# Kernel tuning notes

Measured on AMD Instinct MI355X. Metric: run time of the kernel, lower is better.

The kernel has to match this reference:

```python
import jax, jax.numpy as jnp
import numpy as np

B, NPG = 128, 128          # graphs, nodes per graph
N = B * NPG                # total nodes
K = 16                     # kNN neighbors within cutoff
D = 256                    # embedding_depth
H, DH = 4, 32              # heads = num_layers, head dim = (D//2)//H
L = 4                      # num graph convolutions
NR = 50                    # num_radial
CUTOFF = 2.0
OUT = 3 + 100              # 3 + max_ntypes


def setup_inputs() -> dict:
    rng = np.random.default_rng(0)
    pos = rng.standard_normal((N, 3)).astype(np.float32)
    nbrs = np.zeros((N, K), np.int32)
    mask = np.zeros((N, K), np.float32)
    for g in range(B):  # per-graph kNN with radial cutoff (setup only, numpy)
        p = pos[g * NPG:(g + 1) * NPG]
        d2 = ((p[:, None, :] - p[None, :, :]) ** 2).sum(-1)
        np.fill_diagonal(d2, np.inf)
        idx = np.argsort(d2, axis=1)[:, :K]
        dk = np.sqrt(np.take_along_axis(d2, idx, 1))
        nbrs[g * NPG:(g + 1) * NPG] = idx + g * NPG
        mask[g * NPG:(g + 1) * NPG] = (dk <= CUTOFF).astype(np.float32)
    batch_idx = np.repeat(np.arange(B, dtype=np.int32), NPG)

    key = jax.random.key(0)
    ks = jax.random.split(key, 12)
    s = 0.02
    return {
        'encoding': jax.random.normal(ks[0], (B, D), jnp.float32),
        'pos': jnp.asarray(pos),
        'batch_idx': jnp.asarray(batch_idx),
        'neighbors': jnp.asarray(nbrs),
        'nbr_mask': jnp.asarray(mask),
        'W_in': jax.random.normal(ks[1], (D + 3, D), jnp.float32) * s,
        'b_in': jnp.zeros((D,), jnp.float32),
        'Wq': jax.random.normal(ks[2], (L, D, H * DH), jnp.float32) * s,
        'Wk': jax.random.normal(ks[3], (L, D, H * DH), jnp.float32) * s,
        'Wv': jax.random.normal(ks[4], (L, D, H * DH), jnp.float32) * s,
        'We': jax.random.normal(ks[5], (L, NR, H * DH), jnp.float32) * s,
        'Wo': jax.random.normal(ks[6], (L, H * DH, D), jnp.float32) * s,
        'bo': jnp.zeros((L, D), jnp.float32),
        'Wfc': jax.random.normal(ks[7], (L, D, D), jnp.float32) * s,
        'bfc': jnp.zeros((L, D), jnp.float32),
        'ln_g': jnp.ones((L, D), jnp.float32),
        'ln_b': jnp.zeros((L, D), jnp.float32),
        'W_out': jax.random.normal(ks[8], (D, OUT), jnp.float32) * s,
        'b_out': jnp.zeros((OUT,), jnp.float32),
    }


def reference(encoding, pos, batch_idx, neighbors, nbr_mask,
              W_in, b_in, Wq, Wk, Wv, We, Wo, bo, Wfc, bfc,
              ln_g, ln_b, W_out, b_out):
    # x = encoding.repeat_interleave(graph_sizes); x[:, 0] = 1
    x = encoding[batch_idx]                      # [N, D]
    x = x.at[:, 0].set(1.0)
    h = jnp.concatenate([x, pos], axis=-1) @ W_in + b_in   # concat pos, embed

    # gaussian radial basis of neighbor distances
    dvec = pos[neighbors] - pos[:, None, :]      # [N, K, 3]
    d = jnp.sqrt((dvec ** 2).sum(-1) + 1e-12)    # [N, K]
    centers = jnp.linspace(0.0, CUTOFF, NR)
    width = centers[1] - centers[0]
    rbf = jnp.exp(-0.5 * ((d[..., None] - centers) / width) ** 2)  # [N, K, NR]

    scale = 1.0 / jnp.sqrt(jnp.float32(DH))
    m = nbr_mask[..., None]                      # [N, K, 1]
    for l in range(L):                           # TransformerConv layers
        q = (h @ Wq[l]).reshape(N, H, DH)
        k = (h @ Wk[l]).reshape(N, H, DH)
        v = (h @ Wv[l]).reshape(N, H, DH)
        e = (rbf @ We[l]).reshape(N, K, H, DH)   # edge embedding
        kj = k[neighbors] + e                    # [N, K, H, DH]
        vj = v[neighbors] + e
        logits = jnp.einsum('nhd,nkhd->nkh', q, kj) * scale
        logits = jnp.where(m > 0, logits, -1e9)
        a = jax.nn.softmax(logits, axis=1) * m   # masked attention over K
        msg = jnp.einsum('nkh,nkhd->nhd', a, vj).reshape(N, H * DH)
        h = h + msg @ Wo[l] + bo[l]              # residual update
        mu = h.mean(-1, keepdims=True)
        var = h.var(-1, keepdims=True)
        h = ln_g[l] * (h - mu) / jnp.sqrt(var + 1e-5) + ln_b[l]
        h = jax.nn.gelu(h @ Wfc[l] + bfc[l])     # nodewise fc (1 layer)

    return h @ W_out + b_out                     # [N, 3 + max_ntypes]
```

## Files before the change

### kernel.cpp

```cpp
#include <hip/hip_runtime.h>
#include <hip/hip_bf16.h>
#include <math.h>

#define N_PTS 16384
#define NLAYER 4

typedef __attribute__((ext_vector_type(8))) short bfrag;
typedef __attribute__((ext_vector_type(4))) float f32x4;
typedef __attribute__((ext_vector_type(4))) unsigned short u16x4;
typedef unsigned short ushort_t;
typedef unsigned int uint_t;

__device__ __forceinline__ ushort_t f2b(float f) {
  __hip_bfloat16 h = __float2bfloat16(f);
  return *reinterpret_cast<const ushort_t*>(&h);
}
__device__ __forceinline__ float b2f(ushort_t u) {
  union { uint_t i; float f; } c; c.i = ((uint_t)u) << 16; return c.f;
}
__device__ __forceinline__ float blo(uint_t u) {
  union { uint_t i; float f; } c; c.i = u << 16; return c.f;
}
__device__ __forceinline__ float bhi(uint_t u) {
  union { uint_t i; float f; } c; c.i = u & 0xffff0000u; return c.f;
}

__device__ __forceinline__ void gload16(const ushort_t* g, ushort_t* l) {
  __builtin_amdgcn_global_load_lds(
      (const __attribute__((address_space(1))) unsigned int*)g,
      (__attribute__((address_space(3))) unsigned int*)l, 16, 0, 0);
}

__global__ __launch_bounds__(256) void base_kernel(
    const float* __restrict__ enc, const float* __restrict__ W_in,
    const float* __restrict__ b_in, float* __restrict__ base)
{
  int b = blockIdx.x, j = threadIdx.x;
  __shared__ float se[256];
  se[j] = enc[b * 256 + j];
  __syncthreads();
  float acc = b_in[j] + W_in[j];
  for (int i = 1; i < 256; ++i) acc += se[i] * W_in[i * 256 + j];
  base[b * 256 + j] = acc;
}

__global__ __launch_bounds__(256) void embed_kernel(
    const float* __restrict__ base, const int* __restrict__ batch_idx,
    const float* __restrict__ pos, const float* __restrict__ W_in,
    float* __restrict__ h, ushort_t* __restrict__ h_bf)
{
  int n = blockIdx.x, j = threadIdx.x;
  int b = batch_idx[n];
  float px = pos[n * 3 + 0], py = pos[n * 3 + 1], pz = pos[n * 3 + 2];
  float v = base[b * 256 + j]
      + px * W_in[256 * 256 + j] + py * W_in[257 * 256 + j] + pz * W_in[258 * 256 + j];
  h[(size_t)n * 256 + j] = v;
  h_bf[(size_t)n * 256 + j] = f2b(v);
}

__global__ __launch_bounds__(256) void prep_qkv(
    const float* __restrict__ Wq, const float* __restrict__ Wk,
    const float* __restrict__ Wv, const float* __restrict__ We,
    ushort_t* __restrict__ out)
{
  int idx = blockIdx.x * 256 + threadIdx.x;
  int l = idx / (640 * 256);
  int rem = idx - l * (640 * 256);
  int j = rem >> 8, k = rem & 255;
  float v = 0.f;
  if (j < 128) v = Wq[((size_t)l * 256 + k) * 128 + j];
  else if (j < 328) {
    int p = j - 128, hq = p / 50, r = p - hq * 50;
    const float* wq = &Wq[((size_t)l * 256 + k) * 128 + hq * 32];
    const float* we = &We[((size_t)l * 50 + r) * 128 + hq * 32];
#pragma unroll
    for (int d = 0; d < 32; ++d) v += wq[d] * we[d];
  } else if (j < 456) v = Wk[((size_t)l * 256 + k) * 128 + (j - 328)];
  else if (j < 584) v = Wv[((size_t)l * 256 + k) * 128 + (j - 456)];
  out[idx] = f2b(v);
}

__global__ __launch_bounds__(256) void prep_bcat(
    const float* __restrict__ We, const float* __restrict__ Wo, ushort_t* __restrict__ out)
{
  int idx = blockIdx.x * 256 + threadIdx.x;
  int l = idx / (256 * 384);
  int rem = idx - l * (256 * 384);
  int j = rem / 384, k2 = rem - j * 384;
  float v = 0.f;
  if (k2 < 128) v = Wo[((size_t)l * 128 + k2) * 256 + j];
  else if (k2 < 328) {
    int p = k2 - 128, hq = p / 50, r = p - hq * 50;
    const float* we = &We[((size_t)l * 50 + r) * 128 + hq * 32];
    const float* wo = &Wo[((size_t)l * 128 + hq * 32) * 256 + j];
#pragma unroll
    for (int d = 0; d < 32; ++d) v += we[d] * wo[(size_t)d * 256];
  }
  out[idx] = f2b(v);
}

__global__ __launch_bounds__(256) void prep_wfc(
    const float* __restrict__ Wfc, ushort_t* __restrict__ out)
{
  int idx = blockIdx.x * 256 + threadIdx.x;
  int l = idx >> 16, rem = idx & 65535;
  int j = rem >> 8, k = rem & 255;
  out[idx] = f2b(Wfc[((size_t)l * 256 + k) * 256 + j]);
}

__global__ __launch_bounds__(256) void prep_wout(
    const float* __restrict__ W_out, ushort_t* __restrict__ out)
{
  int idx = blockIdx.x * 256 + threadIdx.x;
  int j = idx >> 8, k = idx & 255;
  out[idx] = (j < 103) ? f2b(W_out[(size_t)k * 103 + j]) : (ushort_t)0;
}

template<int MODE>
__global__ __launch_bounds__(512, 2) void fused_layer(
    const ushort_t* __restrict__ A0,
    const ushort_t* __restrict__ BcT,
    const float* __restrict__ bo,
    float* __restrict__ h,
    const float* __restrict__ lg, const float* __restrict__ lb,
    const ushort_t* __restrict__ WfT,
    const float* __restrict__ bfc,
    const ushort_t* __restrict__ W3T,
    const float* __restrict__ b3,
    ushort_t* __restrict__ qext_b, ushort_t* __restrict__ kvb,
    float* __restrict__ outF)
{
  __shared__ __align__(16) ushort_t R0[64 * 392];
  __shared__ __align__(16) ushort_t R12[64 * 264 + 256 * 64];
  __shared__ float pS[8][64], pSS[8][64];
  ushort_t* sA  = R0;
  ushort_t* sHg = R0;
  ushort_t* sH  = R12;
  ushort_t* sB  = R12 + 64 * 264;
  ushort_t* B3  = R12;

  const int tid = threadIdx.x;
  const int lane = tid & 63, w = tid >> 6;
  const int l15 = lane & 15, l4 = lane >> 4;
  const int m0 = blockIdx.x * 64;
  const int swzk = (l15 & 7) << 3;

  f32x4 acc[4][2];

  if constexpr (MODE != 2) {
    for (int i = tid; i < 64 * 48; i += 512) {
      int r = i / 48, cc = (i - r * 48) * 8;
      uint4 v = (uint4){0, 0, 0, 0};
      if (cc < 352) v = *(const uint4*)(A0 + (size_t)(m0 + r) * 352 + cc);
      *(uint4*)(&sA[r * 392 + cc]) = v;
    }

#pragma unroll
    for (int m = 0; m < 4; ++m) {
      acc[m][0] = (f32x4){0.f, 0.f, 0.f, 0.f};
      acc[m][1] = (f32x4){0.f, 0.f, 0.f, 0.f};
    }
    for (int ks = 0; ks < 6; ++ks) {
      const int k0 = ks * 64;
#pragma unroll
      for (int it = 0; it < 4; ++it) {
        int chunk = it * 512 + tid;
        int row = chunk >> 3;
        int kc = ((chunk & 7) << 3) ^ ((row & 7) << 3);
        gload16(BcT + (size_t)row * 384 + k0 + kc, sB + (size_t)(it * 512 + w * 64) * 8);
      }
      __syncthreads();
#pragma unroll
      for (int kk = 0; kk < 64; kk += 32) {
        bfrag af[4], bf[2];
#pragma unroll
        for (int m = 0; m < 4; ++m)
          af[m] = *(const bfrag*)(sA + (m * 16 + l15) * 392 + k0 + kk + l4 * 8);
#pragma unroll
        for (int nn = 0; nn < 2; ++nn) {
          int row = w * 32 + nn * 16 + l15;
          bf[nn] = *(const bfrag*)(sB + row * 64 + ((kk + l4 * 8) ^ swzk));
        }
#pragma unroll
        for (int m = 0; m < 4; ++m)
#pragma unroll
          for (int nn = 0; nn < 2; ++nn)
            acc[m][nn] = __builtin_amdgcn_mfma_f32_16x16x32_bf16(af[m], bf[nn], acc[m][nn], 0, 0, 0);
      }
      __syncthreads();
    }

    {
      const int c0 = w * 32 + l15, c1 = c0 + 16;
      const float bo0 = bo[c0], bo1 = bo[c1];
#pragma unroll
      for (int m = 0; m < 4; ++m)
#pragma unroll
        for (int i = 0; i < 4; ++i) {
          const int rl = m * 16 + l4 * 4 + i;
          const size_t r = (size_t)(m0 + rl);
          float x0 = acc[m][0][i] + bo0 + h[r * 256 + c0];
          float x1 = acc[m][1][i] + bo1 + h[r * 256 + c1];
          acc[m][0][i] = x0; acc[m][1][i] = x1;
          float s = x0 + x1, ss = x0 * x0 + x1 * x1;
          s += __shfl_xor(s, 1, 64); ss += __shfl_xor(ss, 1, 64);
          s += __shfl_xor(s, 2, 64); ss += __shfl_xor(ss, 2, 64);
          s += __shfl_xor(s, 4, 64); ss += __shfl_xor(ss, 4, 64);
          s += __shfl_xor(s, 8, 64); ss += __shfl_xor(ss, 8, 64);
          if (l15 == 0) { pS[w][rl] = s; pSS[w][rl] = ss; }
        }
      __syncthreads();
      const float g0 = lg[c0], g1 = lg[c1];
      const float b0 = lb[c0], b1 = lb[c1];
#pragma unroll
      for (int m = 0; m < 4; ++m)
#pragma unroll
        for (int i = 0; i < 4; ++i) {
          const int rl = m * 16 + l4 * 4 + i;
          float s = 0.f, ss = 0.f;
#pragma unroll
          for (int w2 = 0; w2 < 8; ++w2) { s += pS[w2][rl]; ss += pSS[w2][rl]; }
          float mu = s * (1.f / 256.f);
          float var = ss * (1.f / 256.f) - mu * mu;
          float inv = 1.0f / sqrtf(var + 1e-5f);
          sH[rl * 264 + c0] = f2b(g0 * (acc[m][0][i] - mu) * inv + b0);
          sH[rl * 264 + c1] = f2b(g1 * (acc[m][1][i] - mu) * inv + b1);
        }
    }

#pragma unroll
    for (int m = 0; m < 4; ++m) {
      acc[m][0] = (f32x4){0.f, 0.f, 0.f, 0.f};
      acc[m][1] = (f32x4){0.f, 0.f, 0.f, 0.f};
    }
    for (int ks = 0; ks < 4; ++ks) {
      const int k0 = ks * 64;
#pragma unroll
      for (int it = 0; it < 4; ++it) {
        int chunk = it * 512 + tid;
        int row = chunk >> 3;
        int kc = ((chunk & 7) << 3) ^ ((row & 7) << 3);
        gload16(WfT + (size_t)row * 256 + k0 + kc, sB + (size_t)(it * 512 + w * 64) * 8);
      }
      __syncthreads();
#pragma unroll
      for (int kk = 0; kk < 64; kk += 32) {
        bfrag af[4], bf[2];
#pragma unroll
        for (int m = 0; m < 4; ++m)
          af[m] = *(const bfrag*)(sH + (m * 16 + l15) * 264 + k0 + kk + l4 * 8);
#pragma unroll
        for (int nn = 0; nn < 2; ++nn) {
          int row = w * 32 + nn * 16 + l15;
          bf[nn] = *(const bfrag*)(sB + row * 64 + ((kk + l4 * 8) ^ swzk));
        }
#pragma unroll
        for (int m = 0; m < 4; ++m)
#pragma unroll
          for (int nn = 0; nn < 2; ++nn)
            acc[m][nn] = __builtin_amdgcn_mfma_f32_16x16x32_bf16(af[m], bf[nn], acc[m][nn], 0, 0, 0);
      }
      __syncthreads();
    }

    {
      const int c0 = w * 32 + l15, c1 = c0 + 16;
      const float bf0 = bfc[c0], bf1 = bfc[c1];
#pragma unroll
      for (int m = 0; m < 4; ++m)
#pragma unroll
        for (int i = 0; i < 4; ++i) {
          const int rl = m * 16 + l4 * 4 + i;
          const size_t r = (size_t)(m0 + rl);
          float x0 = acc[m][0][i] + bf0;
          float x1 = acc[m][1][i] + bf1;
          float t0 = tanhf(0.7978845608028654f * (x0 + 0.044715f * x0 * x0 * x0));
          float t1 = tanhf(0.7978845608028654f * (x1 + 0.044715f * x1 * x1 * x1));
          float gl0 = 0.5f * x0 * (1.f + t0);
          float gl1 = 0.5f * x1 * (1.f + t1);
          h[r * 256 + c0] = gl0;
          h[r * 256 + c1] = gl1;
          sHg[rl * 264 + c0] = f2b(gl0);
          sHg[rl * 264 + c1] = f2b(gl1);
        }
    }
    __syncthreads();
  } else {
    for (int i = tid; i < 64 * 32; i += 512) {
      int r = i >> 5, cc = (i & 31) << 3;
      *(uint4*)(&sHg[r * 264 + cc]) = *(const uint4*)(A0 + (size_t)(m0 + r) * 256 + cc);
    }
    __syncthreads();
  }

  const int NB = (MODE == 1) ? 1 : 5;
  for (int nb = 0; nb < NB; ++nb) {
    if (nb) __syncthreads();
#pragma unroll
    for (int it = 0; it < 8; ++it) {
      int chunk = it * 512 + tid;
      int row = chunk >> 5;
      int kc = ((chunk & 31) << 3) ^ ((row & 7) << 3);
      gload16(W3T + (size_t)(nb * 128 + row) * 256 + kc, B3 + (size_t)(it * 512 + w * 64) * 8);
    }
    __syncthreads();
    f32x4 a3[4];
#pragma unroll
    for (int m = 0; m < 4; ++m) a3[m] = (f32x4){0.f, 0.f, 0.f, 0.f};
#pragma unroll
    for (int k0 = 0; k0 < 256; k0 += 32) {
      bfrag af[4], bf;
#pragma unroll
      for (int m = 0; m < 4; ++m)
        af[m] = *(const bfrag*)(sHg + (m * 16 + l15) * 264 + k0 + l4 * 8);
      {
        int row = w * 16 + l15;
        bf = *(const bfrag*)(B3 + row * 256 + ((k0 + l4 * 8) ^ swzk));
      }
#pragma unroll
      for (int m = 0; m < 4; ++m)
        a3[m] = __builtin_amdgcn_mfma_f32_16x16x32_bf16(af[m], bf, a3[m], 0, 0, 0);
    }
    const int c = nb * 128 + w * 16 + l15;
#pragma unroll
    for (int m = 0; m < 4; ++m)
#pragma unroll
      for (int i = 0; i < 4; ++i) {
        const size_t r = (size_t)(m0 + m * 16 + l4 * 4 + i);
        float v = a3[m][i];
        if constexpr (MODE == 1) {
          if (c < 103) outF[r * 103 + c] = v + b3[c];
        } else {
          if (c < 328) qext_b[r * 352 + c] = f2b(v);
          else if (c < 584) kvb[r * 256 + (c - 328)] = f2b(v);
        }
      }
  }
}

__global__ __launch_bounds__(256) void attn_kernel(
    const ushort_t* __restrict__ qext, const ushort_t* __restrict__ kvb,
    const float* __restrict__ pos, const int* __restrict__ nbrs,
    const float* __restrict__ mask, ushort_t* __restrict__ Amsg)
{
  __shared__ __align__(16) ushort_t sQ[4][128];
  __shared__ __align__(16) float    sQE[4][4][52];
  __shared__ __align__(16) ushort_t sRbf[4][16][52];
  __shared__ float sA[4][64];
  __shared__ float sD[4][16];
  __shared__ float sMk[4][16];
  __shared__ int   sNb[4][16];

  const int tid = threadIdx.x;
  const int lane = tid & 63, w = tid >> 6;
  const int g = blockIdx.x & 127, q4 = blockIdx.x >> 7;
  const int kk = lane >> 2, hh = lane & 3;

  for (int it = 0; it < 4; ++it) {
    const int n = g * 128 + q4 * 16 + w * 4 + it;
    if (lane < 16) {
      int nb = nbrs[n * 16 + lane];
      sNb[w][lane] = nb;
      sMk[w][lane] = mask[n * 16 + lane];
      float dx = pos[nb * 3 + 0] - pos[n * 3 + 0];
      float dy = pos[nb * 3 + 1] - pos[n * 3 + 1];
      float dz = pos[nb * 3 + 2] - pos[n * 3 + 2];
      sD[w][lane] = sqrtf(dx * dx + dy * dy + dz * dz + 1e-12f);
      sRbf[w][lane][50] = 0; sRbf[w][lane][51] = 0;
      *(uint4*)(&sQ[w][lane * 8]) = *(const uint4*)(qext + (size_t)n * 352 + lane * 8);
    }
    if (lane < 50) {
      uint2 u = *(const uint2*)(qext + (size_t)n * 352 + 128 + lane * 4);
      int p = lane * 4;
#pragma unroll
      for (int e = 0; e < 4; ++e) {
        ushort_t bb = ((const ushort_t*)&u)[e];
        int pp = p + e, h2 = pp / 50, r = pp - h2 * 50;
        sQE[w][h2][r] = b2f(bb);
      }
    }
    if (lane < 8) sQE[w][lane >> 1][50 + (lane & 1)] = 0.f;
    {
      int kk2 = lane & 15;
      float dk = sD[w][kk2];
      int r0 = lane >> 4;
#pragma unroll
      for (int j = 0; j < 13; ++j) {
        int r = r0 + j * 4;
        if (r < 50) {
          float t = (dk - (2.f / 49.f) * (float)r) * 24.5f;
          sRbf[w][kk2][r] = f2b(__expf(-0.5f * t * t));
        }
      }
    }
    const int nb = sNb[w][kk];
    const ushort_t* krow = kvb + (size_t)nb * 256 + hh * 32;
    float qk = 0.f;
#pragma unroll
    for (int c8 = 0; c8 < 4; ++c8) {
      uint4 kv4 = *(const uint4*)(krow + c8 * 8);
      const uint_t* q4p = (const uint_t*)(&sQ[w][hh * 32 + c8 * 8]);
      uint_t qa = q4p[0], qb = q4p[1], qc = q4p[2], qd = q4p[3];
      qk += blo(qa) * blo(kv4.x) + bhi(qa) * bhi(kv4.x)
          + blo(qb) * blo(kv4.y) + bhi(qb) * bhi(kv4.y)
          + blo(qc) * blo(kv4.z) + bhi(qc) * bhi(kv4.z)
          + blo(qd) * blo(kv4.w) + bhi(qd) * bhi(kv4.w);
    }
    float qe = 0.f;
#pragma unroll
    for (int c = 0; c < 13; ++c) {
      float4 qv = *(const float4*)(&sQE[w][hh][c * 4]);
      uint2 rv = *(const uint2*)(&sRbf[w][kk][c * 4]);
      qe += qv.x * blo(rv.x) + qv.y * bhi(rv.x)
          + qv.z * blo(rv.y) + qv.w * bhi(rv.y);
    }
    float lg = 0.17677669529663687f * (qk + qe);
    lg = (sMk[w][kk] > 0.f) ? lg : -1e9f;

    float mx = lg;
#pragma unroll
    for (int off = 4; off < 64; off <<= 1) mx = fmaxf(mx, __shfl_xor(mx, off, 64));
    float ex = __expf(lg - mx);
    float sm = ex;
#pragma unroll
    for (int off = 4; off < 64; off <<= 1) sm += __shfl_xor(sm, off, 64);
    sA[w][kk * 4 + hh] = ex / sm * sMk[w][kk];

    if (lane < 50) {
      float r0 = 0.f, r1 = 0.f, r2 = 0.f, r3 = 0.f;
#pragma unroll
      for (int k2 = 0; k2 < 16; ++k2) {
        float rb = b2f(sRbf[w][k2][lane]);
        r0 += sA[w][k2 * 4 + 0] * rb;
        r1 += sA[w][k2 * 4 + 1] * rb;
        r2 += sA[w][k2 * 4 + 2] * rb;
        r3 += sA[w][k2 * 4 + 3] * rb;
      }
      Amsg[(size_t)n * 352 + 128 + 0 * 50 + lane] = f2b(r0);
      Amsg[(size_t)n * 352 + 128 + 1 * 50 + lane] = f2b(r1);
      Amsg[(size_t)n * 352 + 128 + 2 * 50 + lane] = f2b(r2);
      Amsg[(size_t)n * 352 + 128 + 3 * 50 + lane] = f2b(r3);
    }
    {
      const int h2 = lane >> 4;
      float m0v = 0.f, m1v = 0.f;
#pragma unroll
      for (int k2 = 0; k2 < 16; ++k2) {
        int nb2 = sNb[w][k2];
        uint_t vv = *(const uint_t*)(kvb + (size_t)nb2 * 256 + 128 + lane * 2);
        float a = sA[w][k2 * 4 + h2];
        m0v += a * blo(vv);
        m1v += a * bhi(vv);
      }
      uint_t o = (uint_t)f2b(m0v) | ((uint_t)f2b(m1v) << 16);
      *(uint_t*)(&Amsg[(size_t)n * 352 + lane * 2]) = o;
    }
    if (lane < 24) Amsg[(size_t)n * 352 + 328 + lane] = 0;
  }
}

extern "C" void kernel_launch(void* const* d_in, const int* in_sizes, int n_in,
                              void* d_out, int out_size, void* d_ws, size_t ws_size,
                              hipStream_t stream) {
  const float* enc    = (const float*)d_in[0];
  const float* pos    = (const float*)d_in[1];
  const int*   bidx   = (const int*)  d_in[2];
  const int*   nbrs   = (const int*)  d_in[3];
  const float* mask   = (const float*)d_in[4];
  const float* W_in   = (const float*)d_in[5];
  const float* b_in   = (const float*)d_in[6];
  const float* Wq     = (const float*)d_in[7];
  const float* Wk     = (const float*)d_in[8];
  const float* Wv     = (const float*)d_in[9];
  const float* We     = (const float*)d_in[10];
  const float* Wo     = (const float*)d_in[11];
  const float* bo     = (const float*)d_in[12];
  const float* Wfc    = (const float*)d_in[13];
  const float* bfc    = (const float*)d_in[14];
  const float* ln_g   = (const float*)d_in[15];
  const float* ln_b   = (const float*)d_in[16];
  const float* W_out  = (const float*)d_in[17];
  const float* b_out  = (const float*)d_in[18];
  float* out = (float*)d_out;

  const int N = N_PTS;
  float* ws = (float*)d_ws;
  float*    h      = ws;
  ushort_t* qext_b = (ushort_t*)(h + (size_t)N * 256);
  ushort_t* kvb    = qext_b + (size_t)N * 352;
  ushort_t* h_bf   = kvb + (size_t)N * 256;
  ushort_t* Amsg   = h_bf + (size_t)N * 256;
  float*    base   = (float*)(Amsg + (size_t)N * 352);
  ushort_t* WqkvT  = (ushort_t*)(base + 128 * 256);
  ushort_t* BcT    = WqkvT + 4 * 640 * 256;
  ushort_t* WfT    = BcT  + 4 * 256 * 384;
  ushort_t* WoT    = WfT  + 4 * 256 * 256;

  base_kernel<<<128, 256, 0, stream>>>(enc, W_in, b_in, base);
  embed_kernel<<<N, 256, 0, stream>>>(base, bidx, pos, W_in, h, h_bf);
  prep_qkv<<<(4 * 640 * 256) / 256, 256, 0, stream>>>(Wq, Wk, Wv, We, WqkvT);
  prep_bcat<<<(4 * 256 * 384) / 256, 256, 0, stream>>>(We, Wo, BcT);
  prep_wfc<<<(4 * 256 * 256) / 256, 256, 0, stream>>>(Wfc, WfT);
  prep_wout<<<(128 * 256) / 256, 256, 0, stream>>>(W_out, WoT);

  fused_layer<2><<<N / 64, 512, 0, stream>>>(
      h_bf, nullptr, nullptr, nullptr, nullptr, nullptr, nullptr, nullptr,
      WqkvT, nullptr, qext_b, kvb, nullptr);

  for (int l = 0; l < NLAYER; ++l) {
    const ushort_t* BcT_l = BcT + (size_t)l * 256 * 384;
    const ushort_t* WfT_l = WfT + (size_t)l * 256 * 256;
    const float* bo_l  = bo  + (size_t)l * 256;
    const float* bfc_l = bfc + (size_t)l * 256;
    const float* lg_l  = ln_g + (size_t)l * 256;
    const float* lb_l  = ln_b + (size_t)l * 256;

    attn_kernel<<<1024, 256, 0, stream>>>(qext_b, kvb, pos, nbrs, mask, Amsg);

    if (l < NLAYER - 1) {
      const ushort_t* Wqkv_next = WqkvT + (size_t)(l + 1) * 640 * 256;
      fused_layer<0><<<N / 64, 512, 0, stream>>>(
          Amsg, BcT_l, bo_l, h, lg_l, lb_l, WfT_l, bfc_l,
          Wqkv_next, nullptr, qext_b, kvb, nullptr);
    } else {
      fused_layer<1><<<N / 64, 512, 0, stream>>>(
          Amsg, BcT_l, bo_l, h, lg_l, lb_l, WfT_l, bfc_l,
          WoT, b_out, nullptr, nullptr, out);
    }
  }
}
```

Before: 359.7 us.

## Halve fused_layer row tile and stream weights directly from global into registers

The fused layer kernel now handles 32 rows per block instead of 64 and doubles the grid. Weight tiles are no longer staged in LDS through global_load_lds with per-slice barriers; each wave reads its B fragments straight from global memory (through L2) into registers. LDS shrinks to XOR-swizzled A/H buffers, and the launch bound now asks for 4 blocks per CU to raise occupancy. The trade is twice as much weight traffic per output row and global-memory latency on the MFMA operands, in return for fewer barriers and more concurrent blocks.

```diff
diff --git a/kernel.cpp b/kernel.cpp
--- a/kernel.cpp
+++ b/kernel.cpp
@@ -7,7 +7,6 @@
 
 typedef __attribute__((ext_vector_type(8))) short bfrag;
 typedef __attribute__((ext_vector_type(4))) float f32x4;
-typedef __attribute__((ext_vector_type(4))) unsigned short u16x4;
 typedef unsigned short ushort_t;
 typedef unsigned int uint_t;
 
@@ -23,12 +22,6 @@
 }
 __device__ __forceinline__ float bhi(uint_t u) {
   union { uint_t i; float f; } c; c.i = u & 0xffff0000u; return c.f;
-}
-
-__device__ __forceinline__ void gload16(const ushort_t* g, ushort_t* l) {
-  __builtin_amdgcn_global_load_lds(
-      (const __attribute__((address_space(1))) unsigned int*)g,
-      (__attribute__((address_space(3))) unsigned int*)l, 16, 0, 0);
 }
 
 __global__ __launch_bounds__(256) void base_kernel(
@@ -117,7 +110,7 @@
 }
 
 template<int MODE>
-__global__ __launch_bounds__(512, 2) void fused_layer(
+__global__ __launch_bounds__(512, 4) void fused_layer(
     const ushort_t* __restrict__ A0,
     const ushort_t* __restrict__ BcT,
     const float* __restrict__ bo,
@@ -130,71 +123,54 @@
     ushort_t* __restrict__ qext_b, ushort_t* __restrict__ kvb,
     float* __restrict__ outF)
 {
-  __shared__ __align__(16) ushort_t R0[64 * 392];
-  __shared__ __align__(16) ushort_t R12[64 * 264 + 256 * 64];
-  __shared__ float pS[8][64], pSS[8][64];
-  ushort_t* sA  = R0;
-  ushort_t* sHg = R0;
-  ushort_t* sH  = R12;
-  ushort_t* sB  = R12 + 64 * 264;
-  ushort_t* B3  = R12;
+  __shared__ __align__(16) ushort_t sA[32 * 384];
+  __shared__ __align__(16) ushort_t sH[32 * 256];
+  __shared__ float pS[8][32], pSS[8][32];
 
   const int tid = threadIdx.x;
   const int lane = tid & 63, w = tid >> 6;
   const int l15 = lane & 15, l4 = lane >> 4;
-  const int m0 = blockIdx.x * 64;
-  const int swzk = (l15 & 7) << 3;
-
-  f32x4 acc[4][2];
+  const int m0 = blockIdx.x * 32;
+  const int r7 = l15 & 7;
+
+  f32x4 acc[2][2];
 
   if constexpr (MODE != 2) {
-    for (int i = tid; i < 64 * 48; i += 512) {
-      int r = i / 48, cc = (i - r * 48) * 8;
+    for (int i = tid; i < 32 * 48; i += 512) {
+      int r = i / 48, c8 = i - r * 48;
       uint4 v = (uint4){0, 0, 0, 0};
-      if (cc < 352) v = *(const uint4*)(A0 + (size_t)(m0 + r) * 352 + cc);
-      *(uint4*)(&sA[r * 392 + cc]) = v;
-    }
-
-#pragma unroll
-    for (int m = 0; m < 4; ++m) {
+      if (c8 < 44) v = *(const uint4*)(A0 + (size_t)(m0 + r) * 352 + c8 * 8);
+      *(uint4*)(&sA[r * 384 + ((c8 ^ (r & 7)) << 3)]) = v;
+    }
+    __syncthreads();
+
+#pragma unroll
+    for (int m = 0; m < 2; ++m) {
       acc[m][0] = (f32x4){0.f, 0.f, 0.f, 0.f};
       acc[m][1] = (f32x4){0.f, 0.f, 0.f, 0.f};
     }
-    for (int ks = 0; ks < 6; ++ks) {
-      const int k0 = ks * 64;
-#pragma unroll
-      for (int it = 0; it < 4; ++it) {
-        int chunk = it * 512 + tid;
-        int row = chunk >> 3;
-        int kc = ((chunk & 7) << 3) ^ ((row & 7) << 3);
-        gload16(BcT + (size_t)row * 384 + k0 + kc, sB + (size_t)(it * 512 + w * 64) * 8);
-      }
-      __syncthreads();
-#pragma unroll
-      for (int kk = 0; kk < 64; kk += 32) {
-        bfrag af[4], bf[2];
-#pragma unroll
-        for (int m = 0; m < 4; ++m)
-          af[m] = *(const bfrag*)(sA + (m * 16 + l15) * 392 + k0 + kk + l4 * 8);
-#pragma unroll
-        for (int nn = 0; nn < 2; ++nn) {
-          int row = w * 32 + nn * 16 + l15;
-          bf[nn] = *(const bfrag*)(sB + row * 64 + ((kk + l4 * 8) ^ swzk));
-        }
-#pragma unroll
-        for (int m = 0; m < 4; ++m)
-#pragma unroll
-          for (int nn = 0; nn < 2; ++nn)
-            acc[m][nn] = __builtin_amdgcn_mfma_f32_16x16x32_bf16(af[m], bf[nn], acc[m][nn], 0, 0, 0);
-      }
-      __syncthreads();
-    }
-
-    {
-      const int c0 = w * 32 + l15, c1 = c0 + 16;
+    {
+      const ushort_t* bB0 = BcT + (size_t)(w * 32 + l15) * 384 + l4 * 8;
+      const ushort_t* bB1 = bB0 + 16 * 384;
+#pragma unroll
+      for (int k0 = 0; k0 < 352; k0 += 32) {
+        const int ch = (k0 >> 3) + l4;
+        bfrag a0 = *(const bfrag*)(sA + (0 * 16 + l15) * 384 + ((ch ^ r7) << 3));
+        bfrag a1 = *(const bfrag*)(sA + (1 * 16 + l15) * 384 + ((ch ^ r7) << 3));
+        bfrag b0 = *(const bfrag*)(bB0 + k0);
+        bfrag b1 = *(const bfrag*)(bB1 + k0);
+        acc[0][0] = __builtin_amdgcn_mfma_f32_16x16x32_bf16(a0, b0, acc[0][0], 0, 0, 0);
+        acc[0][1] = __builtin_amdgcn_mfma_f32_16x16x32_bf16(a0, b1, acc[0][1], 0, 0, 0);
+        acc[1][0] = __builtin_amdgcn_mfma_f32_16x16x32_bf16(a1, b0, acc[1][0], 0, 0, 0);
+        acc[1][1] = __builtin_amdgcn_mfma_f32_16x16x32_bf16(a1, b1, acc[1][1], 0, 0, 0);
+      }
+    }
+
+    const int c0 = w * 32 + l15, c1 = c0 + 16;
+    {
       const float bo0 = bo[c0], bo1 = bo[c1];
 #pragma unroll
-      for (int m = 0; m < 4; ++m)
+      for (int m = 0; m < 2; ++m)
 #pragma unroll
         for (int i = 0; i < 4; ++i) {
           const int rl = m * 16 + l4 * 4 + i;
@@ -209,11 +185,14 @@
           s += __shfl_xor(s, 8, 64); ss += __shfl_xor(ss, 8, 64);
           if (l15 == 0) { pS[w][rl] = s; pSS[w][rl] = ss; }
         }
-      __syncthreads();
+    }
+    __syncthreads();
+    {
       const float g0 = lg[c0], g1 = lg[c1];
       const float b0 = lb[c0], b1 = lb[c1];
-#pragma unroll
-      for (int m = 0; m < 4; ++m)
+      const int ch0 = c0 >> 3, ch1 = c1 >> 3;
+#pragma unroll
+      for (int m = 0; m < 2; ++m)
 #pragma unroll
         for (int i = 0; i < 4; ++i) {
           const int rl = m * 16 + l4 * 4 + i;
@@ -223,51 +202,41 @@
           float mu = s * (1.f / 256.f);
           float var = ss * (1.f / 256.f) - mu * mu;
           float inv = 1.0f / sqrtf(var + 1e-5f);
-          sH[rl * 264 + c0] = f2b(g0 * (acc[m][0][i] - mu) * inv + b0);
-          sH[rl * 264 + c1] = f2b(g1 * (acc[m][1][i] - mu) * inv + b1);
+          sH[rl * 256 + (((ch0 ^ (rl & 7)) << 3) | (c0 & 7))] =
+              f2b(g0 * (acc[m][0][i] - mu) * inv + b0);
+          sH[rl * 256 + (((ch1 ^ (rl & 7)) << 3) | (c1 & 7))] =
+              f2b(g1 * (acc[m][1][i] - mu) * inv + b1);
         }
     }
-
-#pragma unroll
-    for (int m = 0; m < 4; ++m) {
+    __syncthreads();
+
+#pragma unroll
+    for (int m = 0; m < 2; ++m) {
       acc[m][0] = (f32x4){0.f, 0.f, 0.f, 0.f};
       acc[m][1] = (f32x4){0.f, 0.f, 0.f, 0.f};
     }
-    for (int ks = 0; ks < 4; ++ks) {
-      const int k0 = ks * 64;
-#pragma unroll
-      for (int it = 0; it < 4; ++it) {
-        int chunk = it * 512 + tid;
-        int row = chunk >> 3;
-        int kc = ((chunk & 7) << 3) ^ ((row & 7) << 3);
-        gload16(WfT + (size_t)row * 256 + k0 + kc, sB + (size_t)(it * 512 + w * 64) * 8);
-      }
-      __syncthreads();
-#pragma unroll
-      for (int kk = 0; kk < 64; kk += 32) {
-        bfrag af[4], bf[2];
-#pragma unroll
-        for (int m = 0; m < 4; ++m)
-          af[m] = *(const bfrag*)(sH + (m * 16 + l15) * 264 + k0 + kk + l4 * 8);
-#pragma unroll
-        for (int nn = 0; nn < 2; ++nn) {
-          int row = w * 32 + nn * 16 + l15;
-          bf[nn] = *(const bfrag*)(sB + row * 64 + ((kk + l4 * 8) ^ swzk));
-        }
-#pragma unroll
-        for (int m = 0; m < 4; ++m)
-#pragma unroll
-          for (int nn = 0; nn < 2; ++nn)
-            acc[m][nn] = __builtin_amdgcn_mfma_f32_16x16x32_bf16(af[m], bf[nn], acc[m][nn], 0, 0, 0);
-      }
-      __syncthreads();
-    }
-
-    {
-      const int c0 = w * 32 + l15, c1 = c0 + 16;
+    {
+      const ushort_t* bB0 = WfT + (size_t)(w * 32 + l15) * 256 + l4 * 8;
+      const ushort_t* bB1 = bB0 + 16 * 256;
+#pragma unroll
+      for (int k0 = 0; k0 < 256; k0 += 32) {
+        const int ch = (k0 >> 3) + l4;
+        bfrag a0 = *(const bfrag*)(sH + (0 * 16 + l15) * 256 + ((ch ^ r7) << 3));
+        bfrag a1 = *(const bfrag*)(sH + (1 * 16 + l15) * 256 + ((ch ^ r7) << 3));
+        bfrag b0 = *(const bfrag*)(bB0 + k0);
+        bfrag b1 = *(const bfrag*)(bB1 + k0);
+        acc[0][0] = __builtin_amdgcn_mfma_f32_16x16x32_bf16(a0, b0, acc[0][0], 0, 0, 0);
+        acc[0][1] = __builtin_amdgcn_mfma_f32_16x16x32_bf16(a0, b1, acc[0][1], 0, 0, 0);
+        acc[1][0] = __builtin_amdgcn_mfma_f32_16x16x32_bf16(a1, b0, acc[1][0], 0, 0, 0);
+        acc[1][1] = __builtin_amdgcn_mfma_f32_16x16x32_bf16(a1, b1, acc[1][1], 0, 0, 0);
+      }
+    }
+
+    {
       const float bf0 = bfc[c0], bf1 = bfc[c1];
-#pragma unroll
-      for (int m = 0; m < 4; ++m)
+      const int ch0 = c0 >> 3, ch1 = c1 >> 3;
+#pragma unroll
+      for (int m = 0; m < 2; ++m)
 #pragma unroll
         for (int i = 0; i < 4; ++i) {
           const int rl = m * 16 + l4 * 4 + i;
@@ -280,50 +249,38 @@
           float gl1 = 0.5f * x1 * (1.f + t1);
           h[r * 256 + c0] = gl0;
           h[r * 256 + c1] = gl1;
-          sHg[rl * 264 + c0] = f2b(gl0);
-          sHg[rl * 264 + c1] = f2b(gl1);
+          sA[rl * 256 + (((ch0 ^ (rl & 7)) << 3) | (c0 & 7))] = f2b(gl0);
+          sA[rl * 256 + (((ch1 ^ (rl & 7)) << 3) | (c1 & 7))] = f2b(gl1);
         }
     }
     __syncthreads();
   } else {
-    for (int i = tid; i < 64 * 32; i += 512) {
-      int r = i >> 5, cc = (i & 31) << 3;
-      *(uint4*)(&sHg[r * 264 + cc]) = *(const uint4*)(A0 + (size_t)(m0 + r) * 256 + cc);
+    for (int i = tid; i < 32 * 32; i += 512) {
+      int r = i >> 5, c8 = i & 31;
+      *(uint4*)(&sA[r * 256 + ((c8 ^ (r & 7)) << 3)]) =
+          *(const uint4*)(A0 + (size_t)(m0 + r) * 256 + c8 * 8);
     }
     __syncthreads();
   }
 
   const int NB = (MODE == 1) ? 1 : 5;
   for (int nb = 0; nb < NB; ++nb) {
-    if (nb) __syncthreads();
-#pragma unroll
-    for (int it = 0; it < 8; ++it) {
-      int chunk = it * 512 + tid;
-      int row = chunk >> 5;
-      int kc = ((chunk & 31) << 3) ^ ((row & 7) << 3);
-      gload16(W3T + (size_t)(nb * 128 + row) * 256 + kc, B3 + (size_t)(it * 512 + w * 64) * 8);
-    }
-    __syncthreads();
-    f32x4 a3[4];
-#pragma unroll
-    for (int m = 0; m < 4; ++m) a3[m] = (f32x4){0.f, 0.f, 0.f, 0.f};
+    f32x4 a3[2];
+    a3[0] = (f32x4){0.f, 0.f, 0.f, 0.f};
+    a3[1] = (f32x4){0.f, 0.f, 0.f, 0.f};
+    const ushort_t* bB = W3T + (size_t)(nb * 128 + w * 16 + l15) * 256 + l4 * 8;
 #pragma unroll
     for (int k0 = 0; k0 < 256; k0 += 32) {
-      bfrag af[4], bf;
-#pragma unroll
-      for (int m = 0; m < 4; ++m)
-        af[m] = *(const bfrag*)(sHg + (m * 16 + l15) * 264 + k0 + l4 * 8);
-      {
-        int row = w * 16 + l15;
-        bf = *(const bfrag*)(B3 + row * 256 + ((k0 + l4 * 8) ^ swzk));
-      }
-#pragma unroll
-      for (int m = 0; m < 4; ++m)
-        a3[m] = __builtin_amdgcn_mfma_f32_16x16x32_bf16(af[m], bf, a3[m], 0, 0, 0);
+      const int ch = (k0 >> 3) + l4;
+      bfrag a0 = *(const bfrag*)(sA + (0 * 16 + l15) * 256 + ((ch ^ r7) << 3));
+      bfrag a1 = *(const bfrag*)(sA + (1 * 16 + l15) * 256 + ((ch ^ r7) << 3));
+      bfrag b0 = *(const bfrag*)(bB + k0);
+      a3[0] = __builtin_amdgcn_mfma_f32_16x16x32_bf16(a0, b0, a3[0], 0, 0, 0);
+      a3[1] = __builtin_amdgcn_mfma_f32_16x16x32_bf16(a1, b0, a3[1], 0, 0, 0);
     }
     const int c = nb * 128 + w * 16 + l15;
 #pragma unroll
-    for (int m = 0; m < 4; ++m)
+    for (int m = 0; m < 2; ++m)
 #pragma unroll
       for (int i = 0; i < 4; ++i) {
         const size_t r = (size_t)(m0 + m * 16 + l4 * 4 + i);
@@ -503,7 +460,7 @@
   prep_wfc<<<(4 * 256 * 256) / 256, 256, 0, stream>>>(Wfc, WfT);
   prep_wout<<<(128 * 256) / 256, 256, 0, stream>>>(W_out, WoT);
 
-  fused_layer<2><<<N / 64, 512, 0, stream>>>(
+  fused_layer<2><<<N / 32, 512, 0, stream>>>(
       h_bf, nullptr, nullptr, nullptr, nullptr, nullptr, nullptr, nullptr,
       WqkvT, nullptr, qext_b, kvb, nullptr);
 
@@ -519,11 +476,11 @@
 
     if (l < NLAYER - 1) {
       const ushort_t* Wqkv_next = WqkvT + (size_t)(l + 1) * 640 * 256;
-      fused_layer<0><<<N / 64, 512, 0, stream>>>(
+      fused_layer<0><<<N / 32, 512, 0, stream>>>(
           Amsg, BcT_l, bo_l, h, lg_l, lb_l, WfT_l, bfc_l,
           Wqkv_next, nullptr, qext_b, kvb, nullptr);
     } else {
-      fused_layer<1><<<N / 64, 512, 0, stream>>>(
+      fused_layer<1><<<N / 32, 512, 0, stream>>>(
           Amsg, BcT_l, bo_l, h, lg_l, lb_l, WfT_l, bfc_l,
           WoT, b_out, nullptr, nullptr, out);
     }
```

Measured after the change: 330.3 us. -8.2%, faster.
